# Performance work log

Measured on AMD Instinct MI355X. Metric: run time of the kernel, lower is better.

## Reference

```python
import jax, jax.numpy as jnp
import numpy as np

N, E, H, C, IN = 20000, 640000, 4, 64, 256
HC = H * C
NEG_SLOPE = 0.2


def setup_inputs() -> dict:
    key = jax.random.key(0)
    ks = jax.random.split(key, 24)
    rn = lambda k, s: jax.random.normal(k, s, jnp.float32) * 0.05
    return {
        "x": jax.random.normal(ks[0], (N, IN), jnp.float32),
        "edge_index": jax.random.randint(ks[1], (2, E), 0, N),
        "confidence": jax.random.normal(ks[2], (N,), jnp.float32),
        "w_in": rn(ks[3], (IN, C)), "b_in": jnp.zeros((C,), jnp.float32),
        "lin_w0": rn(ks[4], (C, HC)),
        "lin_w12": rn(ks[5], (2, HC, HC)),
        "att_src": rn(ks[6], (3, H, C)),
        "att_dst": rn(ks[7], (3, H, C)),
        "gat_bias": jnp.zeros((3, HC), jnp.float32),
        "conf_w": rn(ks[8], (HC, 1)), "conf_b": jnp.zeros((1,), jnp.float32),
        "nc_w1": rn(ks[9], (HC, C)), "nc_b1": jnp.zeros((C,), jnp.float32),
        "nc_w2": rn(ks[10], (C, 1)), "nc_b2": jnp.zeros((1,), jnp.float32),
        "oc_w1": rn(ks[11], (HC, C)), "oc_b1": jnp.zeros((C,), jnp.float32),
        "oc_w2": rn(ks[12], (C, 1)), "oc_b2": jnp.zeros((1,), jnp.float32),
        "ec_w1": rn(ks[13], (HC, C)), "ec_b1": jnp.zeros((C,), jnp.float32),
        "ec_w2": rn(ks[14], (C, 4)), "ec_b2": jnp.zeros((4,), jnp.float32),
    }


def _gat_layer(h_in, src, dst, n, lin_w, a_src, a_dst, bias):
    # h_in: (n, in_ch). PyG GATConv: linear -> per-edge attn -> segment softmax -> scatter-add.
    h = (h_in @ lin_w).reshape(n, H, C)
    s_src = jnp.einsum("nhc,hc->nh", h, a_src)  # (n, H)
    s_dst = jnp.einsum("nhc,hc->nh", h, a_dst)
    alpha = jax.nn.leaky_relu(s_src[src] + s_dst[dst], NEG_SLOPE)  # (E', H)
    # softmax over incoming edges of each dst node (self-loops guarantee coverage)
    amax = jax.ops.segment_max(alpha, dst, num_segments=n)
    ex = jnp.exp(alpha - amax[dst])
    denom = jax.ops.segment_sum(ex, dst, num_segments=n)
    coef = ex / jnp.maximum(denom[dst], 1e-16)
    msg = h[src] * coef[:, :, None]  # (E', H, C)
    out = jax.ops.segment_sum(msg, dst, num_segments=n)
    return out.reshape(n, HC) + bias


def reference(x, edge_index, confidence, w_in, b_in, lin_w0, lin_w12,
              att_src, att_dst, gat_bias, conf_w, conf_b,
              nc_w1, nc_b1, nc_w2, nc_b2, oc_w1, oc_b1, oc_w2, oc_b2,
              ec_w1, ec_b1, ec_w2, ec_b2):
    n = x.shape[0]
    loops = jnp.arange(n)
    src = jnp.concatenate([edge_index[0], loops])  # PyG add_self_loops=True
    dst = jnp.concatenate([edge_index[1], loops])
    h = jax.nn.relu(x @ w_in + b_in)  # input_proj + relu (dropout off in eval)
    lin_ws = [lin_w0, lin_w12[0], lin_w12[1]]
    conf_norm = jax.nn.sigmoid(confidence)  # (n,)
    for i in range(3):
        h_new = _gat_layer(h, src, dst, n, lin_ws[i], att_src[i], att_dst[i], gat_bias[i])
        cw = jax.nn.sigmoid(h_new @ conf_w + conf_b)[:, 0] * conf_norm
        h_new = h_new * cw[:, None]
        h = h + h_new if h.shape[-1] == h_new.shape[-1] else h_new
        if i < 2:
            h = jax.nn.relu(h)
    mlp = lambda w1, b1, w2, b2: jax.nn.relu(h @ w1 + b1) @ w2 + b2
    node_pred = jax.nn.sigmoid(mlp(nc_w1, nc_b1, nc_w2, nc_b2))[:, 0]
    origin_pred = jax.nn.sigmoid(mlp(oc_w1, oc_b1, oc_w2, oc_b2))[:, 0]
    error_type_pred = mlp(ec_w1, ec_b1, ec_w2, ec_b2)
    return node_pred, origin_pred, error_type_pred, h
```

## Files before the change

kernel.cpp:

```cpp
#include <hip/hip_runtime.h>
#include <cstdint>
#include <cstddef>

#define NN   20000
#define NPAD 20224
#define EE   640000
#define E2   660000
#define HHD  4
#define CC   64
#define HC   256
#define NEG  0.2f

typedef short bf16x8 __attribute__((ext_vector_type(8)));
typedef float f32x4 __attribute__((ext_vector_type(4)));

__device__ __forceinline__ float sigmoidf_(float x) { return 1.0f / (1.0f + __expf(-x)); }

__device__ __forceinline__ float wred_sum(float v) {
#pragma unroll
    for (int d = 32; d; d >>= 1) v += __shfl_xor(v, d, 64);
    return v;
}

__device__ __forceinline__ unsigned short f2bf(float f) {
    unsigned u = __float_as_uint(f);
    u = (u + 0x7fff + ((u >> 16) & 1)) >> 16;
    return (unsigned short)u;
}
__device__ __forceinline__ float bfval(unsigned short h) { return __uint_as_float(((unsigned)h) << 16); }
__device__ __forceinline__ float bf_lo(unsigned u) { return __uint_as_float(u << 16); }
__device__ __forceinline__ float bf_hi(unsigned u) { return __uint_as_float(u & 0xffff0000u); }

__global__ void count_edges(const int* __restrict__ ei, int* __restrict__ cnt) {
    int e = blockIdx.x * 256 + threadIdx.x;
    if (e < E2) {
        int d = (e < EE) ? ei[EE + e] : (e - EE);
        atomicAdd(&cnt[d], 1);
    }
}

__global__ __launch_bounds__(1024) void scan_off(const int* __restrict__ cnt,
                                                 int* __restrict__ off,
                                                 int* __restrict__ cur) {
    __shared__ int buf[1024];
    int t = threadIdx.x;
    int base = t * 20;
    int local[20];
    int s = 0;
#pragma unroll
    for (int i = 0; i < 20; i++) {
        int idx = base + i;
        int v = (idx < NN) ? cnt[idx] : 0;
        local[i] = v;
        s += v;
    }
    buf[t] = s;
    __syncthreads();
    for (int d = 1; d < 1024; d <<= 1) {
        int tv = (t >= d) ? buf[t - d] : 0;
        __syncthreads();
        buf[t] += tv;
        __syncthreads();
    }
    int run = buf[t] - s;
#pragma unroll
    for (int i = 0; i < 20; i++) {
        int idx = base + i;
        if (idx < NN) { off[idx] = run; cur[idx] = run; }
        run += local[i];
    }
    if (t == 1023) off[NN] = buf[1023];
}

__global__ void scatter_edges(const int* __restrict__ ei, int* __restrict__ cur,
                              int* __restrict__ csr) {
    int e = blockIdx.x * 256 + threadIdx.x;
    if (e < E2) {
        int s, d;
        if (e < EE) { s = ei[e]; d = ei[EE + e]; }
        else        { s = e - EE; d = s; }
        int p = atomicAdd(&cur[d], 1);
        csr[p] = s;
    }
}

#define WTOT 212992
__global__ void prep_inputs(const float* __restrict__ x,
                            const float* __restrict__ w_in, const float* __restrict__ lin_w0,
                            const float* __restrict__ lin_w12,
                            const float* __restrict__ nc1, const float* __restrict__ oc1,
                            const float* __restrict__ ec1,
                            const float* __restrict__ nb, const float* __restrict__ ob,
                            const float* __restrict__ eb,
                            unsigned short* __restrict__ whi,
                            float* __restrict__ bcat,
                            unsigned short* __restrict__ xh, unsigned short* __restrict__ xl) {
    int idx = blockIdx.x * 256 + threadIdx.x;
    if (idx < NN * 64) {
        float4 v = ((const float4*)x)[idx];
        ushort4 hi, lo;
        hi.x = f2bf(v.x); lo.x = f2bf(v.x - bfval(hi.x));
        hi.y = f2bf(v.y); lo.y = f2bf(v.y - bfval(hi.y));
        hi.z = f2bf(v.z); lo.z = f2bf(v.z - bfval(hi.z));
        hi.w = f2bf(v.w); lo.w = f2bf(v.w - bfval(hi.w));
        ((ushort4*)xh)[idx] = hi;
        ((ushort4*)xl)[idx] = lo;
    }
    if (idx < 192) {
        int g = idx >> 6, jj = idx & 63;
        const float* b = (g == 0) ? nb : ((g == 1) ? ob : eb);
        bcat[idx] = b[jj];
    }
    if (idx >= WTOT) return;
    float v;
    if (idx < 16384) {
        int n = idx >> 8, k = idx & 255;
        v = w_in[k * 64 + n];
    } else if (idx < 32768) {
        int r = idx - 16384;
        int n = r >> 6, k = r & 63;
        v = lin_w0[k * 256 + n];
    } else if (idx < 98304) {
        int r = idx - 32768;
        int n = r >> 8, k = r & 255;
        v = lin_w12[k * 256 + n];
    } else if (idx < 163840) {
        int r = idx - 98304;
        int n = r >> 8, k = r & 255;
        v = lin_w12[65536 + k * 256 + n];
    } else {
        int r = idx - 163840;
        int n = r >> 8, k = r & 255;
        int g = n >> 6, jj = n & 63;
        const float* w = (g == 0) ? nc1 : ((g == 1) ? oc1 : ec1);
        v = w[k * 64 + jj];
    }
    whi[idx] = f2bf(v);
}

template <int K, int OUT_CH, int MODE>
__global__ __launch_bounds__(256) void gemm_lds(
    const unsigned short* __restrict__ Ahp, const unsigned short* __restrict__ Alp,
    const unsigned short* __restrict__ Wh,
    const float* __restrict__ bias,
    unsigned short* __restrict__ Outh, unsigned short* __restrict__ Outl,
    const float* __restrict__ a_src, const float* __restrict__ a_dst,
    float* __restrict__ s_src, float* __restrict__ s_dst,
    const float* __restrict__ w2n, const float* __restrict__ w2o,
    const float* __restrict__ w2e,
    const float* __restrict__ b2n, const float* __restrict__ b2o,
    const float* __restrict__ b2e,
    float* __restrict__ outbuf, int nreal) {
    constexpr int LB = K + 8;
    constexpr int NS = K / 32;
    __shared__ unsigned short Bh[64 * LB];
    const int tid = threadIdx.x;
    const int wv = tid >> 6, lane = tid & 63;
    const int quad = lane >> 4, ln = lane & 15;
    const int mb = blockIdx.x * 64;
    const int cb = blockIdx.y * 64;
    const int r0 = mb + wv * 16 + ln;

    const unsigned short* aph = Ahp + (size_t)r0 * K + quad * 8;
    const unsigned short* apl = Alp + (size_t)r0 * K + quad * 8;
    bf16x8 ah[NS], al[NS];
#pragma unroll
    for (int s = 0; s < NS; s++) {
        ah[s] = *(const bf16x8*)(aph + s * 32);
        al[s] = *(const bf16x8*)(apl + s * 32);
    }

    constexpr int NCHK = 64 * (K / 8);
#pragma unroll
    for (int i = 0; i < NCHK / 256; i++) {
        int flat = tid + i * 256;
        int r = flat / (K / 8);
        int c = (flat % (K / 8)) * 8;
        *(uint4*)&Bh[r * LB + c] = *(const uint4*)&Wh[(size_t)(cb + r) * K + c];
    }
    __syncthreads();

    f32x4 acc[4];
#pragma unroll
    for (int j = 0; j < 4; j++) {
        acc[j][0] = 0.f; acc[j][1] = 0.f; acc[j][2] = 0.f; acc[j][3] = 0.f;
    }

#pragma unroll
    for (int s = 0; s < NS; s++) {
#pragma unroll
        for (int cg = 0; cg < 4; cg++) {
            bf16x8 bh = *(const bf16x8*)&Bh[(cg * 16 + ln) * LB + quad * 8 + s * 32];
            acc[cg] = __builtin_amdgcn_mfma_f32_16x16x32_bf16(ah[s], bh, acc[cg], 0, 0, 0);
            acc[cg] = __builtin_amdgcn_mfma_f32_16x16x32_bf16(al[s], bh, acc[cg], 0, 0, 0);
        }
    }

    if (MODE == 1) {
        float av[4], dv[4];
#pragma unroll
        for (int cg = 0; cg < 4; cg++) {
            av[cg] = a_src[cb + cg * 16 + ln];
            dv[cg] = a_dst[cb + cg * 16 + ln];
        }
#pragma unroll
        for (int reg = 0; reg < 4; reg++) {
            float ps = 0.f, pd = 0.f;
#pragma unroll
            for (int cg = 0; cg < 4; cg++) {
                float t = acc[cg][reg];
                ps += t * av[cg];
                pd += t * dv[cg];
            }
#pragma unroll
            for (int d = 1; d < 16; d <<= 1) {
                ps += __shfl_xor(ps, d, 64);
                pd += __shfl_xor(pd, d, 64);
            }
            if (ln == 0) {
                int row = mb + wv * 16 + quad * 4 + reg;
                if (row < nreal) {
                    s_src[row * 4 + blockIdx.y] = ps;
                    s_dst[row * 4 + blockIdx.y] = pd;
                }
            }
        }
    }

    if (MODE == 3) {
        float bv[4];
#pragma unroll
        for (int cg = 0; cg < 4; cg++) bv[cg] = bias[cb + cg * 16 + ln];
        if (blockIdx.y < 2) {
            const float* w2 = (blockIdx.y == 0) ? w2n : w2o;
            float b2 = (blockIdx.y == 0) ? b2n[0] : b2o[0];
            float wv2[4];
#pragma unroll
            for (int cg = 0; cg < 4; cg++) wv2[cg] = w2[cg * 16 + ln];
#pragma unroll
            for (int reg = 0; reg < 4; reg++) {
                float t = 0.f;
#pragma unroll
                for (int cg = 0; cg < 4; cg++) {
                    float tv = fmaxf(acc[cg][reg] + bv[cg], 0.f);
                    t += tv * wv2[cg];
                }
#pragma unroll
                for (int d = 1; d < 16; d <<= 1) t += __shfl_xor(t, d, 64);
                int row = mb + wv * 16 + quad * 4 + reg;
                if (ln == 0 && row < nreal)
                    outbuf[blockIdx.y * NN + row] = sigmoidf_(t + b2);
            }
        } else {
            float4 w4[4];
#pragma unroll
            for (int cg = 0; cg < 4; cg++) w4[cg] = ((const float4*)w2e)[cg * 16 + ln];
#pragma unroll
            for (int reg = 0; reg < 4; reg++) {
                float e0 = 0.f, e1 = 0.f, e2 = 0.f, e3 = 0.f;
#pragma unroll
                for (int cg = 0; cg < 4; cg++) {
                    float tv = fmaxf(acc[cg][reg] + bv[cg], 0.f);
                    e0 += tv * w4[cg].x; e1 += tv * w4[cg].y;
                    e2 += tv * w4[cg].z; e3 += tv * w4[cg].w;
                }
#pragma unroll
                for (int d = 1; d < 16; d <<= 1) {
                    e0 += __shfl_xor(e0, d, 64); e1 += __shfl_xor(e1, d, 64);
                    e2 += __shfl_xor(e2, d, 64); e3 += __shfl_xor(e3, d, 64);
                }
                int row = mb + wv * 16 + quad * 4 + reg;
                if (ln == 0 && row < nreal) {
                    float4 ev = make_float4(e0 + b2e[0], e1 + b2e[1], e2 + b2e[2], e3 + b2e[3]);
                    *(float4*)&outbuf[2 * NN + row * 4] = ev;
                }
            }
        }
        return;
    }

#pragma unroll
    for (int cg = 0; cg < 4; cg++) {
        int col = cb + cg * 16 + ln;
        int rbase = mb + wv * 16 + quad * 4;
#pragma unroll
        for (int reg = 0; reg < 4; reg++) {
            float v = acc[cg][reg];
            int r = rbase + reg;
            if (MODE == 0) {
                v += bias[col]; v = fmaxf(v, 0.f);
                unsigned short hi = f2bf(v);
                Outh[(size_t)r * OUT_CH + col] = hi;
                Outl[(size_t)r * OUT_CH + col] = f2bf(v - bfval(hi));
            } else if (MODE == 1) {
                Outh[(size_t)r * OUT_CH + col] = f2bf(v);
            }
        }
    }
}

__global__ __launch_bounds__(256) void gat_node(const unsigned short* __restrict__ hhb,
                                                const float* __restrict__ s_src,
                                                const float* __restrict__ s_dst,
                                                const int* __restrict__ csr_src,
                                                const int* __restrict__ csr_off,
                                                const float* __restrict__ gbias,
                                                const float* __restrict__ conf_w,
                                                const float* __restrict__ conf_b,
                                                const float* __restrict__ confid,
                                                unsigned short* __restrict__ h_hi,
                                                unsigned short* __restrict__ h_lo,
                                                float* __restrict__ outbuf,
                                                int layer) {
    __shared__ float Lc[4][64];
    __shared__ int   Ls[4][16];
    int wv = threadIdx.x >> 6;
    int lane = threadIdx.x & 63;
    int n = blockIdx.x * 4 + wv;
    int myhead = lane >> 4, slot = lane & 15;
    int off0 = csr_off[n];
    int deg = csr_off[n + 1] - off0;
    const int* cp = csr_src + off0;
    const unsigned short* hrow = hhb + lane * 4;
    float sdm = s_dst[n * 4 + myhead];

    float ax = 0.f, ay = 0.f, az = 0.f, aw = 0.f, smp = 0.f;
    int nch = (deg + 15) >> 4;
    bool valid = slot < deg;
    int sl = cp[valid ? slot : deg - 1];
    float ssv = s_src[sl * 4 + myhead];
    for (int t = 0; t < nch; t++) {
        float a = ssv + sdm;
        a = a > 0.f ? a : NEG * a;
        float c = valid ? __expf(a) : 0.f;
        smp += c;
        Lc[wv][lane] = c;
        if (myhead == 0) Ls[wv][slot] = sl;
        __builtin_amdgcn_wave_barrier();
        float4 c0 = *(const float4*)&Lc[wv][myhead * 16 + 0];
        float4 c1 = *(const float4*)&Lc[wv][myhead * 16 + 4];
        float4 c2 = *(const float4*)&Lc[wv][myhead * 16 + 8];
        float4 c3 = *(const float4*)&Lc[wv][myhead * 16 + 12];
        int4 s0 = *(const int4*)&Ls[wv][0];
        int4 s1 = *(const int4*)&Ls[wv][4];
        int4 s2 = *(const int4*)&Ls[wv][8];
        int4 s3 = *(const int4*)&Ls[wv][12];
        __builtin_amdgcn_wave_barrier();
        if (t + 1 < nch) {
            int i = ((t + 1) << 4) + slot;
            valid = i < deg;
            sl = cp[valid ? i : deg - 1];
            ssv = s_src[sl * 4 + myhead];
        }
        float cf[16] = {c0.x, c0.y, c0.z, c0.w, c1.x, c1.y, c1.z, c1.w,
                        c2.x, c2.y, c2.z, c2.w, c3.x, c3.y, c3.z, c3.w};
        int sv[16] = {s0.x, s0.y, s0.z, s0.w, s1.x, s1.y, s1.z, s1.w,
                      s2.x, s2.y, s2.z, s2.w, s3.x, s3.y, s3.z, s3.w};
#pragma unroll
        for (int q = 0; q < 16; q++) {
            uint2 u = *(const uint2*)(hrow + ((size_t)sv[q] << 8));
            ax += cf[q] * bf_lo(u.x); ay += cf[q] * bf_hi(u.x);
            az += cf[q] * bf_lo(u.y); aw += cf[q] * bf_hi(u.y);
        }
    }
    smp += __shfl_xor(smp, 1, 64);
    smp += __shfl_xor(smp, 2, 64);
    smp += __shfl_xor(smp, 4, 64);
    smp += __shfl_xor(smp, 8, 64);
    float inv = 1.0f / fmaxf(smp, 1e-16f);
    ax *= inv; ay *= inv; az *= inv; aw *= inv;

    float4 b4 = *(const float4*)&gbias[lane * 4];
    float hx = ax + b4.x, hy = ay + b4.y, hz = az + b4.z, hw = aw + b4.w;
    float4 cw4 = *(const float4*)&conf_w[lane * 4];
    float local = hx * cw4.x + hy * cw4.y + hz * cw4.z + hw * cw4.w;
    float tot = wred_sum(local);
    float cw = sigmoidf_(tot + conf_b[0]) * sigmoidf_(confid[n]);
    hx *= cw; hy *= cw; hz *= cw; hw *= cw;
    if (layer > 0) {
        ushort4 ph = *(const ushort4*)&h_hi[(size_t)n * HC + lane * 4];
        ushort4 pl = *(const ushort4*)&h_lo[(size_t)n * HC + lane * 4];
        hx += bfval(ph.x) + bfval(pl.x);
        hy += bfval(ph.y) + bfval(pl.y);
        hz += bfval(ph.z) + bfval(pl.z);
        hw += bfval(ph.w) + bfval(pl.w);
    }
    if (layer < 2) {
        hx = fmaxf(hx, 0.f); hy = fmaxf(hy, 0.f);
        hz = fmaxf(hz, 0.f); hw = fmaxf(hw, 0.f);
    } else {
        *(float4*)&outbuf[6 * NN + (size_t)n * HC + lane * 4] =
            make_float4(hx, hy, hz, hw);
    }
    ushort4 oh, ol;
    oh.x = f2bf(hx); ol.x = f2bf(hx - bfval(oh.x));
    oh.y = f2bf(hy); ol.y = f2bf(hy - bfval(oh.y));
    oh.z = f2bf(hz); ol.z = f2bf(hz - bfval(oh.z));
    oh.w = f2bf(hw); ol.w = f2bf(hw - bfval(oh.w));
    *(ushort4*)&h_hi[(size_t)n * HC + lane * 4] = oh;
    *(ushort4*)&h_lo[(size_t)n * HC + lane * 4] = ol;
}

extern "C" void kernel_launch(void* const* d_in, const int* in_sizes, int n_in,
                              void* d_out, int out_size, void* d_ws, size_t ws_size,
                              hipStream_t stream) {
    const float* x       = (const float*)d_in[0];
    const int*   ei      = (const int*)d_in[1];
    const float* conf    = (const float*)d_in[2];
    const float* w_in    = (const float*)d_in[3];
    const float* b_in    = (const float*)d_in[4];
    const float* lin_w0  = (const float*)d_in[5];
    const float* lin_w12 = (const float*)d_in[6];
    const float* att_src = (const float*)d_in[7];
    const float* att_dst = (const float*)d_in[8];
    const float* gbias   = (const float*)d_in[9];
    const float* conf_w  = (const float*)d_in[10];
    const float* conf_b  = (const float*)d_in[11];
    const float* nc_w1   = (const float*)d_in[12];
    const float* nc_b1   = (const float*)d_in[13];
    const float* nc_w2   = (const float*)d_in[14];
    const float* nc_b2   = (const float*)d_in[15];
    const float* oc_w1   = (const float*)d_in[16];
    const float* oc_b1   = (const float*)d_in[17];
    const float* oc_w2   = (const float*)d_in[18];
    const float* oc_b2   = (const float*)d_in[19];
    const float* ec_w1   = (const float*)d_in[20];
    const float* ec_b1   = (const float*)d_in[21];
    const float* ec_w2   = (const float*)d_in[22];
    const float* ec_b2   = (const float*)d_in[23];
    float* out = (float*)d_out;

    char* p = (char*)d_ws;
    auto alloc = [&](size_t bytes) -> void* {
        void* r = (void*)p;
        p += (bytes + 255) & ~(size_t)255;
        return r;
    };
    unsigned short* h_hi = (unsigned short*)alloc((size_t)NPAD * HC * 2);
    unsigned short* h_lo = (unsigned short*)alloc((size_t)NPAD * HC * 2);
    unsigned short* hh   = (unsigned short*)alloc((size_t)NPAD * HC * 2);
    unsigned short* h0h  = (unsigned short*)alloc((size_t)NPAD * CC * 2);
    unsigned short* h0l  = (unsigned short*)alloc((size_t)NPAD * CC * 2);
    float*          ssrc = (float*)alloc((size_t)NN * 4 * 4);
    float*          sdst = (float*)alloc((size_t)NN * 4 * 4);
    int*            cnt  = (int*)alloc((size_t)NN * 4);
    int*            off  = (int*)alloc((size_t)(NN + 1) * 4);
    int*            cur  = (int*)alloc((size_t)NN * 4);
    int*            csr  = (int*)alloc((size_t)E2 * 4);
    unsigned short* whi  = (unsigned short*)alloc((size_t)WTOT * 2);
    float*          bcat = (float*)alloc((size_t)192 * 4);
    unsigned short* xh   = (unsigned short*)alloc((size_t)NPAD * 256 * 2 * 2);
    unsigned short* xl   = xh + (size_t)NPAD * 256;

    const unsigned short* wt_in = whi;
    const unsigned short* wt_l0 = whi + 16384;
    const unsigned short* wt_a  = whi + 32768;
    const unsigned short* wt_b  = whi + 98304;
    const unsigned short* wt_hd = whi + 163840;

    hipMemsetAsync(cnt, 0, (size_t)NN * 4, stream);
    count_edges<<<(E2 + 255) / 256, 256, 0, stream>>>(ei, cnt);
    scan_off<<<1, 1024, 0, stream>>>(cnt, off, cur);
    scatter_edges<<<(E2 + 255) / 256, 256, 0, stream>>>(ei, cur, csr);

    prep_inputs<<<(NN * 64 + 255) / 256, 256, 0, stream>>>(
        x, w_in, lin_w0, lin_w12, nc_w1, oc_w1, ec_w1, nc_b1, oc_b1, ec_b1,
        whi, bcat, xh, xl);

    gemm_lds<256, 64, 0><<<dim3(NPAD / 64, 1), 256, 0, stream>>>(
        xh, xl, wt_in, b_in, h0h, h0l, nullptr, nullptr, nullptr, nullptr,
        nullptr, nullptr, nullptr, nullptr, nullptr, nullptr, nullptr, NN);

    gemm_lds<64, 256, 1><<<dim3(NPAD / 64, 4), 256, 0, stream>>>(
        h0h, h0l, wt_l0, nullptr, hh, nullptr, att_src, att_dst, ssrc, sdst,
        nullptr, nullptr, nullptr, nullptr, nullptr, nullptr, nullptr, NN);
    gat_node<<<NN / 4, 256, 0, stream>>>(hh, ssrc, sdst, csr, off, gbias, conf_w, conf_b, conf,
                                         h_hi, h_lo, out, 0);

    for (int i = 1; i < 3; i++) {
        const unsigned short* wh = (i == 1) ? wt_a : wt_b;
        gemm_lds<256, 256, 1><<<dim3(NPAD / 64, 4), 256, 0, stream>>>(
            h_hi, h_lo, wh, nullptr, hh, nullptr,
            att_src + i * HHD * CC, att_dst + i * HHD * CC, ssrc, sdst,
            nullptr, nullptr, nullptr, nullptr, nullptr, nullptr, nullptr, NN);
        gat_node<<<NN / 4, 256, 0, stream>>>(hh, ssrc, sdst, csr, off, gbias + i * HC,
                                             conf_w, conf_b, conf, h_hi, h_lo, out, i);
    }

    gemm_lds<256, 192, 3><<<dim3(NPAD / 64, 3), 256, 0, stream>>>(
        h_hi, h_lo, wt_hd, bcat, nullptr, nullptr, nullptr, nullptr, nullptr, nullptr,
        nc_w2, oc_w2, ec_w2, nc_b2, oc_b2, ec_b2, out, NN);
}
```

Measured before the change: 410.0 us.

## Build CSR via two-level bucketed counting sort with shared-memory atomics

Replaces the global-atomic count/scan/scatter CSR build with a two-pass bucket sort. Edges are first bucketed by destination>>6 using per-block LDS histograms, a global scan and an LDS-cursor scatter into a packed buffer. Each bucket is then sorted locally into the final CSR. This removes the memset and the contended global atomics, and makes the CSR writes more local. The cost is one extra kernel and an extra pass over a packed temp buffer that reuses the xh workspace, which relies on prep_inputs running afterwards.

```diff
diff --git a/kernel.cpp b/kernel.cpp
--- a/kernel.cpp
+++ b/kernel.cpp
@@ -11,6 +11,11 @@
 #define HC   256
 #define NEG  0.2f
 
+#define NBUK 313
+#define NBLK 129
+#define EPB  5120
+#define SCN  (NBUK * NBLK)
+
 typedef short bf16x8 __attribute__((ext_vector_type(8)));
 typedef float f32x4 __attribute__((ext_vector_type(4)));
 
@@ -31,26 +36,36 @@
 __device__ __forceinline__ float bf_lo(unsigned u) { return __uint_as_float(u << 16); }
 __device__ __forceinline__ float bf_hi(unsigned u) { return __uint_as_float(u & 0xffff0000u); }
 
-__global__ void count_edges(const int* __restrict__ ei, int* __restrict__ cnt) {
-    int e = blockIdx.x * 256 + threadIdx.x;
-    if (e < E2) {
-        int d = (e < EE) ? ei[EE + e] : (e - EE);
-        atomicAdd(&cnt[d], 1);
-    }
-}
-
-__global__ __launch_bounds__(1024) void scan_off(const int* __restrict__ cnt,
-                                                 int* __restrict__ off,
-                                                 int* __restrict__ cur) {
+__global__ __launch_bounds__(256) void hist_edges(const int* __restrict__ ei,
+                                                  int* __restrict__ bhist) {
+    __shared__ int h[NBUK];
+    int bl = blockIdx.x, t = threadIdx.x;
+    for (int i = t; i < NBUK; i += 256) h[i] = 0;
+    __syncthreads();
+    int e0 = bl * EPB;
+#pragma unroll 4
+    for (int i = t; i < EPB; i += 256) {
+        int e = e0 + i;
+        if (e < E2) {
+            int d = (e < EE) ? ei[EE + e] : (e - EE);
+            atomicAdd(&h[d >> 6], 1);
+        }
+    }
+    __syncthreads();
+    for (int i = t; i < NBUK; i += 256) bhist[i * NBLK + bl] = h[i];
+}
+
+__global__ __launch_bounds__(1024) void scan_hist(const int* __restrict__ bhist,
+                                                  int* __restrict__ sbase) {
     __shared__ int buf[1024];
     int t = threadIdx.x;
-    int base = t * 20;
-    int local[20];
+    int base = t * 40;
+    int local[40];
     int s = 0;
 #pragma unroll
-    for (int i = 0; i < 20; i++) {
+    for (int i = 0; i < 40; i++) {
         int idx = base + i;
-        int v = (idx < NN) ? cnt[idx] : 0;
+        int v = (idx < SCN) ? bhist[idx] : 0;
         local[i] = v;
         s += v;
     }
@@ -64,23 +79,71 @@
     }
     int run = buf[t] - s;
 #pragma unroll
-    for (int i = 0; i < 20; i++) {
+    for (int i = 0; i < 40; i++) {
         int idx = base + i;
-        if (idx < NN) { off[idx] = run; cur[idx] = run; }
+        if (idx < SCN) sbase[idx] = run;
         run += local[i];
     }
-    if (t == 1023) off[NN] = buf[1023];
-}
-
-__global__ void scatter_edges(const int* __restrict__ ei, int* __restrict__ cur,
-                              int* __restrict__ csr) {
-    int e = blockIdx.x * 256 + threadIdx.x;
-    if (e < E2) {
-        int s, d;
-        if (e < EE) { s = ei[e]; d = ei[EE + e]; }
-        else        { s = e - EE; d = s; }
-        int p = atomicAdd(&cur[d], 1);
-        csr[p] = s;
+}
+
+__global__ __launch_bounds__(256) void scatter_bucket(const int* __restrict__ ei,
+                                                      const int* __restrict__ sbase,
+                                                      unsigned int* __restrict__ ebuf) {
+    __shared__ int cur[NBUK];
+    int bl = blockIdx.x, t = threadIdx.x;
+    for (int i = t; i < NBUK; i += 256) cur[i] = sbase[i * NBLK + bl];
+    __syncthreads();
+    int e0 = bl * EPB;
+#pragma unroll 4
+    for (int i = t; i < EPB; i += 256) {
+        int e = e0 + i;
+        if (e < E2) {
+            int s, d;
+            if (e < EE) { s = ei[e]; d = ei[EE + e]; }
+            else        { s = e - EE; d = s; }
+            int p = atomicAdd(&cur[d >> 6], 1);
+            ebuf[p] = ((unsigned int)(d & 63) << 15) | (unsigned int)s;
+        }
+    }
+}
+
+__global__ __launch_bounds__(256) void build_csr(const unsigned int* __restrict__ ebuf,
+                                                 const int* __restrict__ sbase,
+                                                 int* __restrict__ off,
+                                                 int* __restrict__ csr) {
+    __shared__ int hist[64], sc[64], curl[64];
+    int bu = blockIdx.x, t = threadIdx.x;
+    int base = sbase[bu * NBLK];
+    int end  = (bu + 1 < NBUK) ? sbase[(bu + 1) * NBLK] : E2;
+    int ne = end - base;
+    if (t < 64) hist[t] = 0;
+    __syncthreads();
+    for (int i = t; i < ne; i += 256) {
+        int dl = (int)(ebuf[base + i] >> 15);
+        atomicAdd(&hist[dl], 1);
+    }
+    __syncthreads();
+    if (t < 64) sc[t] = hist[t];
+    __syncthreads();
+    for (int d = 1; d < 64; d <<= 1) {
+        int v = (t < 64 && t >= d) ? sc[t - d] : 0;
+        __syncthreads();
+        if (t < 64) sc[t] += v;
+        __syncthreads();
+    }
+    int n0 = bu * 64;
+    if (t < 64) {
+        int ex = base + sc[t] - hist[t];
+        if (n0 + t < NN) off[n0 + t] = ex;
+        curl[t] = ex;
+    }
+    if (bu == NBUK - 1 && t == 0) off[NN] = E2;
+    __syncthreads();
+    for (int i = t; i < ne; i += 256) {
+        unsigned int v = ebuf[base + i];
+        int dl = (int)(v >> 15);
+        int p = atomicAdd(&curl[dl], 1);
+        csr[p] = (int)(v & 0x7fffu);
     }
 }
 
@@ -443,14 +506,15 @@
     unsigned short* h0l  = (unsigned short*)alloc((size_t)NPAD * CC * 2);
     float*          ssrc = (float*)alloc((size_t)NN * 4 * 4);
     float*          sdst = (float*)alloc((size_t)NN * 4 * 4);
-    int*            cnt  = (int*)alloc((size_t)NN * 4);
     int*            off  = (int*)alloc((size_t)(NN + 1) * 4);
-    int*            cur  = (int*)alloc((size_t)NN * 4);
     int*            csr  = (int*)alloc((size_t)E2 * 4);
+    int*            bhist= (int*)alloc((size_t)SCN * 4);
+    int*            sbase= (int*)alloc((size_t)SCN * 4);
     unsigned short* whi  = (unsigned short*)alloc((size_t)WTOT * 2);
     float*          bcat = (float*)alloc((size_t)192 * 4);
     unsigned short* xh   = (unsigned short*)alloc((size_t)NPAD * 256 * 2 * 2);
     unsigned short* xl   = xh + (size_t)NPAD * 256;
+    unsigned int*   ebuf = (unsigned int*)xh;
 
     const unsigned short* wt_in = whi;
     const unsigned short* wt_l0 = whi + 16384;
@@ -458,10 +522,10 @@
     const unsigned short* wt_b  = whi + 98304;
     const unsigned short* wt_hd = whi + 163840;
 
-    hipMemsetAsync(cnt, 0, (size_t)NN * 4, stream);
-    count_edges<<<(E2 + 255) / 256, 256, 0, stream>>>(ei, cnt);
-    scan_off<<<1, 1024, 0, stream>>>(cnt, off, cur);
-    scatter_edges<<<(E2 + 255) / 256, 256, 0, stream>>>(ei, cur, csr);
+    hist_edges<<<NBLK, 256, 0, stream>>>(ei, bhist);
+    scan_hist<<<1, 1024, 0, stream>>>(bhist, sbase);
+    scatter_bucket<<<NBLK, 256, 0, stream>>>(ei, sbase, ebuf);
+    build_csr<<<NBUK, 256, 0, stream>>>(ebuf, sbase, off, csr);
 
     prep_inputs<<<(NN * 64 + 255) / 256, 256, 0, stream>>>(
         x, w_in, lin_w0, lin_w12, nc_w1, oc_w1, ec_w1, nc_b1, oc_b1, ec_b1,
```

Measured after the change: 391.0 us. 4.6% less time.
